# Optimization experiments

Measured on AMD Instinct MI355X. Metric: run time of the kernel, lower is better.

Reference implementation:

```python
import math
import jax, jax.numpy as jnp
import numpy as np

B, S, D, H, L = 2, 2048, 1024, 16, 4
HD = D // H  # head_dim = 64


def setup_inputs() -> dict:
    key = jax.random.key(0)
    ks = jax.random.split(key, 7)
    scale = 0.02
    return {
        "x": jax.random.normal(ks[0], (B, S, D), jnp.float32),
        "past_q": jax.random.normal(ks[1], (B, H, S, L, HD), jnp.float32),
        "past_v": jax.random.normal(ks[2], (B, H, S, L, HD), jnp.float32),
        "Wq": jax.random.normal(ks[3], (D, D), jnp.float32) * scale,
        "bq": jnp.zeros((D,), jnp.float32),
        "Wo": jax.random.normal(ks[4], (D, D), jnp.float32) * scale,
        "bo": jnp.zeros((D,), jnp.float32),
    }


def reference(x, past_q, past_v, Wq, bq, Wo, bo):
    b, s, d = x.shape
    # q_proj then split heads -> [B,H,S,hd]
    q = (x @ Wq.T + bq).reshape(b, s, H, HD).transpose(0, 2, 1, 3)
    v = x.reshape(b, s, H, HD).transpose(0, 2, 1, 3)
    inv = 1.0 / math.sqrt(HD)
    # token scores: Q used as both query and key, causal mask
    token_scores = jnp.einsum("bhqd,bhkd->bhqk", q, q) * inv
    causal = jnp.triu(jnp.ones((s, s), bool), k=1)
    token_scores = jnp.where(causal, -jnp.inf, token_scores)
    # memory scores: elementwise mul-sum over L cached layers -> [B,H,S,L]
    mem_scores = jnp.einsum("bhsd,bhsld->bhsl", q, past_q) * inv
    scores = jnp.concatenate([token_scores, mem_scores], axis=-1)  # [B,H,S,S+L]
    weights = jax.nn.softmax(scores, axis=-1)
    tw, mw = weights[..., :s], weights[..., s:]
    token_ctx = jnp.einsum("bhqk,bhkd->bhqd", tw, v)
    mem_ctx = jnp.einsum("bhsl,bhsld->bhsd", mw, past_v)
    ctx = (token_ctx + mem_ctx).transpose(0, 2, 1, 3).reshape(b, s, d)
    return jax.nn.gelu(ctx @ Wo.T + bo, approximate=False)
```

## Files before the change

### kernel.cpp

```cpp
#include <hip/hip_runtime.h>
#include <hip/hip_bf16.h>
#include <math.h>

#define S_LEN 2048
#define DIM   1024
#define NH    16
#define NL    4
#define NB    2
#define PARTS_PER_BH 80
#define ALPHA 0.42466086f

typedef __attribute__((ext_vector_type(8))) short bf16x8;
typedef __attribute__((ext_vector_type(4))) float f32x4;
typedef __attribute__((ext_vector_type(4))) unsigned short u16x4;
typedef unsigned short u16;

template <int N> struct Tag { static constexpr int cur = N; };

__device__ __forceinline__ float bf2f(u16 u) {
  union { unsigned int i; float f; } x; x.i = ((unsigned int)u) << 16; return x.f;
}
__device__ __forceinline__ u16 f2bf(float f) {
  union { float f; unsigned int i; } x; x.f = f;
  unsigned int r = x.i + 0x7fffu + ((x.i >> 16) & 1u);
  return (u16)(r >> 16);
}
__device__ __forceinline__ u16 f2bfq(float f) {
  __hip_bfloat16 h = __float2bfloat16(f);
  return *reinterpret_cast<u16*>(&h);
}
__device__ __forceinline__ float ex2(float x) {
  return __builtin_amdgcn_exp2f(x);
}

__device__ __forceinline__ void g2l16(const void* g, void* l) {
  __builtin_amdgcn_global_load_lds(
      (const __attribute__((address_space(1))) void*)g,
      (__attribute__((address_space(3))) void*)l, 16, 0, 0);
}

template <int CTRL>
__device__ __forceinline__ float dppf(float x) {
  union { float f; int i; } u, r;
  u.f = x;
  r.i = __builtin_amdgcn_update_dpp(0, u.i, CTRL, 0xF, 0xF, true);
  return r.f;
}
__device__ __forceinline__ float rsum16(float x) {
  x += dppf<0xB1>(x);
  x += dppf<0x4E>(x);
  x += dppf<0x141>(x);
  x += dppf<0x140>(x);
  return x;
}

__device__ __forceinline__ float gelu_fast(float v) {
  float y = 0.79788456f * (v + 0.044715f * v * v * v);
  float e = ex2(y * 2.88539008f);
  float t = 1.0f - 2.0f / (e + 1.0f);
  return 0.5f * v * (1.0f + t);
}

__global__ __launch_bounds__(256)
void cvt_all(const float* __restrict__ x, const float* __restrict__ wq,
             const float* __restrict__ wo, u16* __restrict__ ox,
             u16* __restrict__ owq, u16* __restrict__ owo, int n4x, int n4w) {
  int i = blockIdx.x * blockDim.x + threadIdx.x;
  const float* src; u16* dst; int j;
  if (i < n4x)            { src = x;  dst = ox;  j = i; }
  else if (i < n4x + n4w) { src = wq; dst = owq; j = i - n4x; }
  else                    { src = wo; dst = owo; j = i - n4x - n4w;
                            if (j >= n4w) return; }
  float4 v = ((const float4*)src)[j];
  ushort4 o;
  o.x = f2bf(v.x); o.y = f2bf(v.y); o.z = f2bf(v.z); o.w = f2bf(v.w);
  ((ushort4*)dst)[j] = o;
}

template <bool GELU, typename OT>
__global__ __launch_bounds__(256)
void gemm_bt(const u16* __restrict__ A, const u16* __restrict__ Bt,
             const float* __restrict__ bias, OT* __restrict__ C,
             int M, int N, int K, float oscale) {
  __shared__ u16 As[2][128 * 64];
  __shared__ u16 Bs[2][64 * 64];
  const int lane = threadIdx.x & 63, wave = threadIdx.x >> 6;
  const int ln = lane & 15, g = lane >> 4;
  const int m0 = blockIdx.y * 128, n0 = blockIdx.x * 64;
  const int wm = wave >> 1, wn = wave & 1;
  f32x4 acc[4][2] = {};

  auto stage = [&](int buf, int k0) {
#pragma unroll
    for (int rd = 0; rd < 6; ++rd) {
      int ch = rd * 4 + wave;
      if (ch < 16) {
        int flatb = ch * 1024 + lane * 16;
        int row = flatb >> 7;
        int within = (flatb & 127) ^ ((row & 7) << 4);
        g2l16((const char*)A + ((size_t)(m0 + row) * K + k0) * 2 + within,
              (char*)As[buf] + ch * 1024);
      } else {
        int flatb = (ch - 16) * 1024 + lane * 16;
        int row = flatb >> 7;
        int within = (flatb & 127) ^ ((row & 7) << 4);
        g2l16((const char*)Bt + ((size_t)(n0 + row) * K + k0) * 2 + within,
              (char*)Bs[buf] + (ch - 16) * 1024);
      }
    }
  };

  stage(0, 0);
  __syncthreads();
  const int NT = K / 64;
  for (int t = 0; t < NT; ++t) {
    const int cur = t & 1;
    if (t + 1 < NT) stage(cur ^ 1, (t + 1) * 64);
#pragma unroll
    for (int kc = 0; kc < 2; ++kc) {
      bf16x8 af[4], bfr[2];
#pragma unroll
      for (int i = 0; i < 4; ++i) {
        int ra = wm * 64 + i * 16 + ln;
        af[i] = *(const bf16x8*)((const char*)As[cur] + ra * 128 +
                                 ((kc * 64 + g * 16) ^ ((ra & 7) << 4)));
      }
#pragma unroll
      for (int j = 0; j < 2; ++j) {
        int rb = wn * 32 + j * 16 + ln;
        bfr[j] = *(const bf16x8*)((const char*)Bs[cur] + rb * 128 +
                                  ((kc * 64 + g * 16) ^ ((rb & 7) << 4)));
      }
#pragma unroll
      for (int i = 0; i < 4; ++i)
#pragma unroll
        for (int j = 0; j < 2; ++j)
          acc[i][j] = __builtin_amdgcn_mfma_f32_16x16x32_bf16(af[i], bfr[j], acc[i][j], 0, 0, 0);
    }
    __syncthreads();
  }

#pragma unroll
  for (int j = 0; j < 2; ++j) {
    int gc = n0 + wn * 32 + j * 16 + ln;
    float bv = bias[gc];
#pragma unroll
    for (int i = 0; i < 4; ++i) {
      int gr0 = m0 + wm * 64 + i * 16 + g * 4;
#pragma unroll
      for (int r = 0; r < 4; ++r) {
        float v = acc[i][j][r] + bv;
        if constexpr (GELU) v = gelu_fast(v);
        v *= oscale;
        if constexpr (sizeof(OT) == 2) C[(size_t)(gr0 + r) * N + gc] = (OT)f2bf(v);
        else                           C[(size_t)(gr0 + r) * N + gc] = (OT)v;
      }
    }
  }
}

__global__ __launch_bounds__(256, 4)
void attn(const u16* __restrict__ Q, const u16* __restrict__ Xb,
          u16* __restrict__ CTXP, float* __restrict__ MP, float* __restrict__ LP) {
  __shared__ __attribute__((aligned(16))) char lds[40960];

  const int lane = threadIdx.x & 63, wave = threadIdx.x >> 6;
  const int ln = lane & 15, g = lane >> 4;
  const int h = blockIdx.y, b = blockIdx.z;

  const int pl = PARTS_PER_BH - 1 - blockIdx.x;
  int qt, chunk;
  if (pl < 8)       { qt = pl;                           chunk = 0; }
  else if (pl < 24) { int i = pl - 8;  qt = 8 + (i >> 1);  chunk = i & 1; }
  else if (pl < 48) { int i = pl - 24; qt = 16 + i / 3;    chunk = i % 3; }
  else              { int i = pl - 48; qt = 24 + (i >> 2); chunk = i & 3; }
  const int len = qt + 1;
  const int parts = (len + 7) >> 3;
  const int kt0 = (chunk * len) / parts;
  const int kt1e = ((chunk + 1) * len) / parts;

  const size_t qrow = (size_t)b * S_LEN + qt * 64 + wave * 16 + ln;
  const bf16x8 qa0 = *(const bf16x8*)(Q + qrow * DIM + h * 64 + g * 8);
  const bf16x8 qa1 = *(const bf16x8*)(Q + qrow * DIM + h * 64 + 32 + g * 8);

  const int tid = threadIdx.x;
  const int vr0 = (tid >> 3) * 2;
  const int vc0 = (tid & 7) * 8;
  const int t7 = tid & 7;
  const int sw7 = (ln & 7) << 4;
  const int kbase0 = ln * 128 + ((g * 16) ^ sw7);
  const int kbase1 = ln * 128 + ((64 + g * 16) ^ sw7);
  const int swb = (ln & 7) ^ (ln >> 3);
  int vrd0[4], vrd1[4];
#pragma unroll
  for (int ns = 0; ns < 4; ++ns) {
    int sw = (swb ^ (ns * 2)) << 4;
    vrd0[ns] = ln * 128 + ((g * 16) ^ sw);
    vrd1[ns] = ln * 128 + ((64 + g * 16) ^ sw);
  }
  int vwr[8];
#pragma unroll
  for (int j = 0; j < 8; ++j)
    vwr[j] = (vc0 + j) * 128 + ((vr0 * 2) ^ ((j ^ t7) << 4));
  int pst[4];
#pragma unroll
  for (int sub = 0; sub < 4; ++sub)
    pst[sub] = 32768 + wave * 2048 + ln * 128 + ((sub * 32 + g * 8) ^ sw7);
  const int prd0 = 32768 + wave * 2048 + ln * 128 + ((g * 16) ^ sw7);
  const int prd1 = 32768 + wave * 2048 + ln * 128 + ((64 + g * 16) ^ sw7);
  int ksrc[2];
#pragma unroll
  for (int rd = 0; rd < 2; ++rd) {
    int ch = rd * 4 + wave;
    int flat = ch * 1024 + lane * 16;
    int row = flat >> 7;
    ksrc[rd] = row * (DIM * 2) + ((flat & 127) ^ ((row & 7) << 4));
  }

  const size_t STEP = (size_t)64 * DIM * 2;
  const char* kq = (const char*)(Q + ((size_t)b * S_LEN + (size_t)kt0 * 64) * DIM + h * 64);
  const char* xv = (const char*)(Xb + ((size_t)b * S_LEN + (size_t)kt0 * 64 + vr0) * DIM + h * 64 + vc0);

  f32x4 acc[4] = {};
  float m_run = -INFINITY;
  float l_run = 0.f;

  {
    bf16x8 r0 = *(const bf16x8*)xv;
    bf16x8 r1 = *(const bf16x8*)(xv + DIM * 2);
#pragma unroll
    for (int rd = 0; rd < 2; ++rd)
      g2l16(kq + ksrc[rd], lds + (rd * 4 + wave) * 1024);
#pragma unroll
    for (int j = 0; j < 8; ++j) {
      unsigned int pack = (unsigned int)(u16)r0[j] | ((unsigned int)(u16)r1[j] << 16);
      *(unsigned int*)(lds + 16384 + vwr[j]) = pack;
    }
  }
  __syncthreads();

  int kt = kt0;
  auto body = [&](auto tag) {
    constexpr int CUR = decltype(tag)::cur;
    constexpr int NXT = CUR ^ 1;
    const bool more = (kt + 1 < kt1e);
    bf16x8 nr0, nr1;
    if (more) {
      const char* nxv = xv + STEP;
      nr0 = *(const bf16x8*)nxv;
      nr1 = *(const bf16x8*)(nxv + DIM * 2);
      const char* nkq = kq + STEP;
#pragma unroll
      for (int rd = 0; rd < 2; ++rd)
        g2l16(nkq + ksrc[rd], lds + NXT * 8192 + (rd * 4 + wave) * 1024);
      __builtin_amdgcn_sched_barrier(0);
    }

    float pv_[4][4];
    __builtin_amdgcn_s_setprio(1);
#pragma unroll
    for (int sub = 0; sub < 4; ++sub) {
      bf16x8 kb0 = *(const bf16x8*)(lds + CUR * 8192 + sub * 2048 + kbase0);
      bf16x8 kb1 = *(const bf16x8*)(lds + CUR * 8192 + sub * 2048 + kbase1);
      f32x4 c = {};
      c = __builtin_amdgcn_mfma_f32_16x16x32_bf16(kb0, qa0, c, 0, 0, 0);
      c = __builtin_amdgcn_mfma_f32_16x16x32_bf16(kb1, qa1, c, 0, 0, 0);
      if (kt == qt) {
#pragma unroll
        for (int r = 0; r < 4; ++r) {
          int key = sub * 16 + g * 4 + r;
          pv_[sub][r] = (key > wave * 16 + ln) ? -INFINITY : c[r];
        }
      } else {
#pragma unroll
        for (int r = 0; r < 4; ++r) pv_[sub][r] = c[r];
      }
    }
    __builtin_amdgcn_s_setprio(0);

    float pmax = pv_[0][0];
#pragma unroll
    for (int sub = 0; sub < 4; ++sub)
#pragma unroll
      for (int r = 0; r < 4; ++r) pmax = fmaxf(pmax, pv_[sub][r]);
    pmax = fmaxf(pmax, __shfl_xor(pmax, 16));
    pmax = fmaxf(pmax, __shfl_xor(pmax, 32));

    if (!__all(pmax <= m_run + 8.0f)) {
      float m_new = fmaxf(m_run, pmax);
      float scl = ex2(m_run - m_new);
      m_run = m_new;
      l_run *= scl;
#pragma unroll
      for (int r = 0; r < 4; ++r) {
        float s = __shfl(scl, g * 4 + r);
#pragma unroll
        for (int ns = 0; ns < 4; ++ns) acc[ns][r] *= s;
      }
    }

    float lsum = 0.f;
#pragma unroll
    for (int sub = 0; sub < 4; ++sub)
#pragma unroll
      for (int r = 0; r < 4; ++r) {
        pv_[sub][r] = ex2(pv_[sub][r] - m_run);
        lsum += pv_[sub][r];
      }
    lsum += __shfl_xor(lsum, 16);
    lsum += __shfl_xor(lsum, 32);
    l_run += lsum;

#pragma unroll
    for (int sub = 0; sub < 4; ++sub) {
      uint2 val;
      val.x = (unsigned int)f2bfq(pv_[sub][0]) | ((unsigned int)f2bfq(pv_[sub][1]) << 16);
      val.y = (unsigned int)f2bfq(pv_[sub][2]) | ((unsigned int)f2bfq(pv_[sub][3]) << 16);
      *(uint2*)(lds + pst[sub]) = val;
    }

    bf16x8 pa0 = *(const bf16x8*)(lds + prd0);
    bf16x8 pa1 = *(const bf16x8*)(lds + prd1);
    __builtin_amdgcn_s_setprio(1);
#pragma unroll
    for (int ns = 0; ns < 4; ++ns) {
      bf16x8 vb0 = *(const bf16x8*)(lds + 16384 + CUR * 8192 + ns * 2048 + vrd0[ns]);
      bf16x8 vb1 = *(const bf16x8*)(lds + 16384 + CUR * 8192 + ns * 2048 + vrd1[ns]);
      acc[ns] = __builtin_amdgcn_mfma_f32_16x16x32_bf16(pa0, vb0, acc[ns], 0, 0, 0);
      acc[ns] = __builtin_amdgcn_mfma_f32_16x16x32_bf16(pa1, vb1, acc[ns], 0, 0, 0);
    }
    __builtin_amdgcn_s_setprio(0);

    if (more) {
#pragma unroll
      for (int j = 0; j < 8; ++j) {
        unsigned int pack = (unsigned int)(u16)nr0[j] | ((unsigned int)(u16)nr1[j] << 16);
        *(unsigned int*)(lds + 16384 + NXT * 8192 + vwr[j]) = pack;
      }
    }
    __syncthreads();
    kq += STEP; xv += STEP;
  };

  for (;;) {
    body(Tag<0>{});
    if (++kt >= kt1e) break;
    body(Tag<1>{});
    if (++kt >= kt1e) break;
  }

  const size_t slot = ((size_t)(b * NH + h)) * PARTS_PER_BH + pl;
#pragma unroll
  for (int ns = 0; ns < 4; ++ns)
#pragma unroll
    for (int r = 0; r < 4; ++r) {
      int qr = wave * 16 + g * 4 + r;
      CTXP[slot * 4096 + (size_t)qr * 64 + ns * 16 + ln] = f2bfq(acc[ns][r]);
    }
  if (lane < 16) {
    MP[slot * 64 + wave * 16 + lane] = m_run;
    LP[slot * 64 + wave * 16 + lane] = l_run;
  }
}

__global__ __launch_bounds__(256)
void finalize(const u16* __restrict__ Q, const float* __restrict__ PQ,
              const float* __restrict__ PV, const u16* __restrict__ CTXP,
              const float* __restrict__ MP, const float* __restrict__ LP,
              u16* __restrict__ Cout) {
  const int lane = threadIdx.x & 63, wave = threadIdx.x >> 6;
  const int g = lane >> 4, li = lane & 15;
  const size_t row = (size_t)blockIdx.x * 4 + wave;
  const int s = (int)(row & (S_LEN - 1));
  const int h = (int)((row >> 11) & (NH - 1));
  const int b = (int)(row >> 15);

  const int qt = s >> 6, G = qt >> 3, parts = G + 1;
  const int baseG[4] = {0, 8, 24, 48};
  const int p0 = baseG[G] + (qt & 7) * parts;
  const size_t slot0 = ((size_t)(b * NH + h)) * PARTS_PER_BH + p0;
  const int sr = s & 63;

  f32x4 pq4 = __builtin_nontemporal_load((const f32x4*)(PQ + row * (NL * 64) + lane * 4));
  f32x4 pv4 = __builtin_nontemporal_load((const f32x4*)(PV + row * (NL * 64) + lane * 4));
  const size_t qoff = ((size_t)b * S_LEN + s) * DIM + h * 64 + li * 4;
  ushort4 qu = *(const ushort4*)(Q + qoff);

  const int cg = (g < parts) ? g : 0;
  float mcg = MP[(slot0 + cg) * 64 + sr];
  float lcg = LP[(slot0 + cg) * 64 + sr];
  ushort4 cu = *(const ushort4*)(CTXP + (slot0 + cg) * 4096 + (size_t)sr * 64 + li * 4);
  if (g >= parts) mcg = -INFINITY;

  float prod = bf2f(qu.x) * pq4.x + bf2f(qu.y) * pq4.y +
               bf2f(qu.z) * pq4.z + bf2f(qu.w) * pq4.w;
  float msc = rsum16(prod) * ALPHA;

  float v = fmaxf(msc, mcg);
  v = fmaxf(v, __shfl_xor(v, 16));
  v = fmaxf(v, __shfl_xor(v, 32));
  const float m_fin = v;

  const float w_tok = ex2(mcg - m_fin);
  const float w_mem = ex2(msc - m_fin);
  float t0 = w_tok * bf2f(cu.x) + w_mem * pv4.x;
  float t1 = w_tok * bf2f(cu.y) + w_mem * pv4.y;
  float t2 = w_tok * bf2f(cu.z) + w_mem * pv4.z;
  float t3 = w_tok * bf2f(cu.w) + w_mem * pv4.w;
  float lw = w_tok * lcg + w_mem;

  t0 += __shfl_xor(t0, 16); t1 += __shfl_xor(t1, 16);
  t2 += __shfl_xor(t2, 16); t3 += __shfl_xor(t3, 16);
  lw += __shfl_xor(lw, 16);
  t0 += __shfl_xor(t0, 32); t1 += __shfl_xor(t1, 32);
  t2 += __shfl_xor(t2, 32); t3 += __shfl_xor(t3, 32);
  lw += __shfl_xor(lw, 32);

  const float inv = 1.0f / lw;
  if (lane < 16) {
    u16x4 o;
    o.x = f2bfq(t0 * inv); o.y = f2bfq(t1 * inv);
    o.z = f2bfq(t2 * inv); o.w = f2bfq(t3 * inv);
    __builtin_nontemporal_store(o, (u16x4*)(Cout + qoff));
  }
}

extern "C" void kernel_launch(void* const* d_in, const int* in_sizes, int n_in,
                              void* d_out, int out_size, void* d_ws, size_t ws_size,
                              hipStream_t stream) {
  const float* x  = (const float*)d_in[0];
  const float* pq = (const float*)d_in[1];
  const float* pv = (const float*)d_in[2];
  const float* Wq = (const float*)d_in[3];
  const float* bq = (const float*)d_in[4];
  const float* Wo = (const float*)d_in[5];
  const float* bo = (const float*)d_in[6];
  float* out = (float*)d_out;

  const int M = NB * S_LEN;
  u16*   Qws  = (u16*)d_ws;
  u16*   Cws  = Qws + (size_t)M * DIM;
  u16*   xbf  = Cws + (size_t)M * DIM;
  u16*   Wqbf = xbf + (size_t)M * DIM;
  u16*   Wobf = Wqbf + (size_t)DIM * DIM;
  u16*   CTXP = Wobf + (size_t)DIM * DIM;
  float* MP   = (float*)(CTXP + (size_t)NB * NH * PARTS_PER_BH * 4096);
  float* LP   = MP + (size_t)NB * NH * PARTS_PER_BH * 64;

  const int n4x = M * DIM / 4, n4w = DIM * DIM / 4;
  cvt_all<<<(n4x + 2 * n4w + 255) / 256, 256, 0, stream>>>(
      x, Wq, Wo, xbf, Wqbf, Wobf, n4x, n4w);

  gemm_bt<false, u16><<<dim3(DIM / 64, M / 128), 256, 0, stream>>>(
      xbf, Wqbf, bq, Qws, M, DIM, DIM, ALPHA);
  attn<<<dim3(PARTS_PER_BH, NH, NB), 256, 0, stream>>>(Qws, xbf, CTXP, MP, LP);
  finalize<<<NB * NH * S_LEN / 4, 256, 0, stream>>>(Qws, pq, pv, CTXP, MP, LP, Cws);
  gemm_bt<true, float><<<dim3(DIM / 64, M / 128), 256, 0, stream>>>(
      Cws, Wobf, bo, out, M, DIM, DIM, 1.0f);
}
```

Before: 121.7 us.

## Fuse memory-score merge into attention for unsplit query tiles, shrink finalize grid

For query tiles whose key range is handled by a single partition (the first 8 tiles per head), the attention kernel now stages its accumulator and softmax stats in LDS. It then applies the past-layer memory scores and values itself and writes the final bf16 context directly. The finalize kernel is launched only over the remaining rows (s >= 512), with its indexing remapped to match. This skips the partial-result round trip through global memory and part of the finalize work. In exchange, those attention blocks take on extra per-row loads of past_q/past_v and a serial 16-row epilogue.

```diff
diff --git a/kernel.cpp b/kernel.cpp
--- a/kernel.cpp
+++ b/kernel.cpp
@@ -161,7 +161,9 @@
 
 __global__ __launch_bounds__(256, 4)
 void attn(const u16* __restrict__ Q, const u16* __restrict__ Xb,
-          u16* __restrict__ CTXP, float* __restrict__ MP, float* __restrict__ LP) {
+          const float* __restrict__ PQ, const float* __restrict__ PV,
+          u16* __restrict__ CTXP, float* __restrict__ MP, float* __restrict__ LP,
+          u16* __restrict__ Cout) {
   __shared__ __attribute__((aligned(16))) char lds[40960];
 
   const int lane = threadIdx.x & 63, wave = threadIdx.x >> 6;
@@ -349,7 +351,66 @@
     if (++kt >= kt1e) break;
   }
 
-  const size_t slot = ((size_t)(b * NH + h)) * PARTS_PER_BH + pl;
+  const size_t bh = (size_t)(b * NH + h);
+
+  if (parts == 1) {
+    float* ctxs  = (float*)lds;
+    float* statm = (float*)(lds + 32768);
+    float* statl = (float*)(lds + 33024);
+#pragma unroll
+    for (int ns = 0; ns < 4; ++ns)
+#pragma unroll
+      for (int r = 0; r < 4; ++r)
+        ctxs[(wave * 16 + g * 4 + r) * 68 + ns * 16 + ln] = acc[ns][r];
+    if (lane < 16) {
+      statm[wave * 16 + lane] = m_run;
+      statl[wave * 16 + lane] = l_run;
+    }
+    __syncthreads();
+
+    for (int rr = 0; rr < 16; ++rr) {
+      const int qv = wave * 16 + rr;
+      const int srow = qt * 64 + qv;
+      const size_t row = (bh << 11) + srow;
+      f32x4 pq4 = __builtin_nontemporal_load((const f32x4*)(PQ + row * (NL * 64) + lane * 4));
+      f32x4 pv4 = __builtin_nontemporal_load((const f32x4*)(PV + row * (NL * 64) + lane * 4));
+      const size_t qoff = ((size_t)b * S_LEN + srow) * DIM + h * 64 + ln * 4;
+      ushort4 qu = *(const ushort4*)(Q + qoff);
+      const float m_tok = statm[qv];
+      const float l_tok = statl[qv];
+      f32x4 cd4 = *(const f32x4*)(ctxs + qv * 68 + ln * 4);
+
+      float prod = bf2f(qu.x) * pq4.x + bf2f(qu.y) * pq4.y +
+                   bf2f(qu.z) * pq4.z + bf2f(qu.w) * pq4.w;
+      float msc = rsum16(prod) * ALPHA;
+      float mx = fmaxf(msc, __shfl_xor(msc, 16));
+      mx = fmaxf(mx, __shfl_xor(mx, 32));
+      const float m_fin = fmaxf(m_tok, mx);
+      const float a = ex2(m_tok - m_fin);
+      const float w_mem = ex2(msc - m_fin);
+
+      float t0 = w_mem * pv4.x, t1 = w_mem * pv4.y;
+      float t2 = w_mem * pv4.z, t3 = w_mem * pv4.w;
+      float lw = w_mem;
+      t0 += __shfl_xor(t0, 16); t1 += __shfl_xor(t1, 16);
+      t2 += __shfl_xor(t2, 16); t3 += __shfl_xor(t3, 16);
+      lw += __shfl_xor(lw, 16);
+      t0 += __shfl_xor(t0, 32); t1 += __shfl_xor(t1, 32);
+      t2 += __shfl_xor(t2, 32); t3 += __shfl_xor(t3, 32);
+      lw += __shfl_xor(lw, 32);
+
+      const float inv = 1.0f / (lw + a * l_tok);
+      if (lane < 16) {
+        u16x4 o;
+        o.x = f2bfq((a * cd4.x + t0) * inv); o.y = f2bfq((a * cd4.y + t1) * inv);
+        o.z = f2bfq((a * cd4.z + t2) * inv); o.w = f2bfq((a * cd4.w + t3) * inv);
+        __builtin_nontemporal_store(o, (u16x4*)(Cout + qoff));
+      }
+    }
+    return;
+  }
+
+  const size_t slot = bh * PARTS_PER_BH + pl;
 #pragma unroll
   for (int ns = 0; ns < 4; ++ns)
 #pragma unroll
@@ -370,15 +431,17 @@
               u16* __restrict__ Cout) {
   const int lane = threadIdx.x & 63, wave = threadIdx.x >> 6;
   const int g = lane >> 4, li = lane & 15;
-  const size_t row = (size_t)blockIdx.x * 4 + wave;
-  const int s = (int)(row & (S_LEN - 1));
-  const int h = (int)((row >> 11) & (NH - 1));
-  const int b = (int)(row >> 15);
+  const int idx = blockIdx.x * 4 + wave;
+  const int bh_i = idx / 1536;
+  const int s = 512 + (idx - bh_i * 1536);
+  const int h = bh_i & (NH - 1);
+  const int b = bh_i >> 4;
+  const size_t row = ((size_t)bh_i << 11) + s;
 
   const int qt = s >> 6, G = qt >> 3, parts = G + 1;
   const int baseG[4] = {0, 8, 24, 48};
   const int p0 = baseG[G] + (qt & 7) * parts;
-  const size_t slot0 = ((size_t)(b * NH + h)) * PARTS_PER_BH + p0;
+  const size_t slot0 = ((size_t)bh_i) * PARTS_PER_BH + p0;
   const int sr = s & 63;
 
   f32x4 pq4 = __builtin_nontemporal_load((const f32x4*)(PQ + row * (NL * 64) + lane * 4));
@@ -453,8 +516,10 @@
 
   gemm_bt<false, u16><<<dim3(DIM / 64, M / 128), 256, 0, stream>>>(
       xbf, Wqbf, bq, Qws, M, DIM, DIM, ALPHA);
-  attn<<<dim3(PARTS_PER_BH, NH, NB), 256, 0, stream>>>(Qws, xbf, CTXP, MP, LP);
-  finalize<<<NB * NH * S_LEN / 4, 256, 0, stream>>>(Qws, pq, pv, CTXP, MP, LP, Cws);
+  attn<<<dim3(PARTS_PER_BH, NH, NB), 256, 0, stream>>>(
+      Qws, xbf, pq, pv, CTXP, MP, LP, Cws);
+  finalize<<<NB * NH * (S_LEN - 512) / 4, 256, 0, stream>>>(
+      Qws, pq, pv, CTXP, MP, LP, Cws);
   gemm_bt<true, float><<<dim3(DIM / 64, M / 128), 256, 0, stream>>>(
       Cws, Wobf, bo, out, M, DIM, DIM, 1.0f);
 }
```

Result: slower. 134.2 us (+10.3%).
